# Optimization experiments

Hardware: AMD Instinct MI355X
Metric: run time of the kernel (lower is better)

Reference implementation:

```python
import jax, jax.numpy as jnp
import numpy as np

N = 400000
IN, H, F, S, OUT = 64, 256, 128, 16, 5


def setup_inputs() -> dict:
    key = jax.random.key(0)
    ks = jax.random.split(key, 20)
    def lin(k, fan_in, fan_out):
        bound = 1.0 / np.sqrt(fan_in)
        kw, kb = jax.random.split(k)
        W = jax.random.uniform(kw, (fan_in, fan_out), jnp.float32, -bound, bound)
        b = jax.random.uniform(kb, (fan_out,), jnp.float32, -bound, bound)
        return W, b
    pw1, pb1 = lin(ks[0], IN, H)
    pw2, pb2 = lin(ks[1], H, H)
    pw3, pb3 = lin(ks[2], H, F)
    rw1, rb1 = lin(ks[3], F, H)
    rw2, rb2 = lin(ks[4], H, H)
    rw3, rb3 = lin(ks[5], H, F)
    w1, b1 = lin(ks[6], F + S, H)
    w2, b2 = lin(ks[7], H, H)
    w3, b3 = lin(ks[8], H, OUT)
    x = jax.random.normal(ks[9], (N, IN), jnp.float32)
    x_static = jax.random.normal(ks[10], (S,), jnp.float32)
    return {
        "x": x, "x_static": x_static,
        "pw1": pw1, "pb1": pb1, "pw2": pw2, "pb2": pb2, "pw3": pw3, "pb3": pb3,
        "rw1": rw1, "rb1": rb1, "rw2": rw2, "rb2": rb2, "rw3": rw3, "rb3": rb3,
        "w1": w1, "b1": b1, "w2": w2, "b2": b2, "w3": w3, "b3": b3,
    }


def reference(x, x_static, pw1, pb1, pw2, pb2, pw3, pb3,
              rw1, rb1, rw2, rb2, rw3, rb3, w1, b1, w2, b2, w3, b3):
    # phi network applied to every row, then sum-pool (DeepSets).
    # Batched matmuls replace the original Python per-row loop; the per-row
    # bias of the final phi Linear is summed N times, matching the loop.
    h = jax.nn.relu(x @ pw1 + pb1)              # [N, H]
    h = jax.nn.relu(h @ pw2 + pb2)              # [N, H]
    phi = h @ pw3 + pb3                          # [N, F]
    fp = jnp.sum(phi, axis=0)                    # [F]
    # rho network
    r = jax.nn.relu(fp @ rw1 + rb1)
    r = jax.nn.relu(r @ rw2 + rb2)
    r = r @ rw3 + rb3                            # [F]
    out = jnp.concatenate([r, x_static], axis=0)  # [F + S]
    out = jax.nn.relu(out @ w1 + b1)
    out = jax.nn.relu(out @ w2 + b2)
    return out @ w3 + b3                          # [OUT]
```

## Files before the change

### kernel.cpp

```cpp
#include <hip/hip_runtime.h>


typedef unsigned short u16;
typedef _Float16 f16x8 __attribute__((ext_vector_type(8)));
typedef _Float16 f16x2 __attribute__((ext_vector_type(2)));
typedef float f32x4 __attribute__((ext_vector_type(4)));
typedef int i32x4 __attribute__((ext_vector_type(4)));

#define NBLK 256

__global__ void prep_kernel(const float* __restrict__ pw1, const float* __restrict__ pw2,
                            _Float16* __restrict__ w1f, _Float16* __restrict__ w2f,
                            float* __restrict__ gsum,
                            const float* __restrict__ pw3, const float* __restrict__ rw1,
                            const float* __restrict__ rw2, const float* __restrict__ rw3,
                            const float* __restrict__ hw1, const float* __restrict__ hw2,
                            const float* __restrict__ hw3) {
    int idx = blockIdx.x * blockDim.x + threadIdx.x;
    if (idx < 256) gsum[idx] = 0.f;
    if (idx < 16384) {
        int j = idx & 7, l = (idx >> 3) & 63, ks = (idx >> 9) & 1, ct = idx >> 10;
        int k = 32 * ks + 8 * (l >> 4) + j;
        int col = 16 * ct + (l & 15);
        w1f[idx] = (_Float16)pw1[k * 256 + col];
    } else {
        int o = idx - 16384;
        int j = o & 7, l = (o >> 3) & 63, ks = (o >> 9) & 7, ct = o >> 12;
        int k = 32 * ks + 8 * (l >> 4) + j;
        int col = 16 * ct + (l & 15);
        w2f[o] = (_Float16)pw2[k * 256 + col];
    }
    float s = 0.f;
    if (idx < 32768) s += pw3[idx];
    if (idx < 32768) s += rw1[idx];
    if (idx < 65536) s += rw2[idx];
    if (idx < 32768) s += rw3[idx];
    if (idx < 36864) s += hw1[idx];
    if (idx < 65536) s += hw2[idx];
    if (idx < 1280)  s += hw3[idx];
    asm volatile("" :: "v"(s));
}

__device__ __forceinline__ void pin_reg(f16x8& v) {
    i32x4 t = __builtin_bit_cast(i32x4, v);
    asm volatile("" : "+v"(t));
    v = __builtin_bit_cast(f16x8, t);
}
__device__ __forceinline__ unsigned pk(float a, float b) {
    return __builtin_bit_cast(unsigned, __builtin_amdgcn_cvt_pkrtz(a, b));
}

__global__ __attribute__((amdgpu_flat_work_group_size(512, 512), amdgpu_waves_per_eu(2, 2)))
void phi_kernel(
    const float* __restrict__ x,
    const float* __restrict__ pb1, const float* __restrict__ pb2,
    const _Float16* __restrict__ w1g, const _Float16* __restrict__ w2g,
    float* __restrict__ gsum, int ntiles) {
    __shared__ __align__(16) u16 xs[2][64 * 64];
    __shared__ __align__(16) u16 h1s[2][64 * 256];

    const int tid = threadIdx.x;
    const int l = tid & 63;
    const int w = tid >> 6;
    const int fr = l & 15;
    const int fg = l >> 4;
    const int wb = w * 32;

    f16x8 w1r[2][2];
#pragma unroll
    for (int ct = 0; ct < 2; ++ct)
#pragma unroll
        for (int ks = 0; ks < 2; ++ks) {
            int ctg = 2 * w + ct;
            w1r[ct][ks] = *(const f16x8*)(w1g + (((ctg << 1) + ks) << 9) + (l << 3));
        }
    f16x8 w2r[2][8];
#pragma unroll
    for (int ct = 0; ct < 2; ++ct)
#pragma unroll
        for (int ks = 0; ks < 8; ++ks) {
            int ctg = 2 * w + ct;
            w2r[ct][ks] = *(const f16x8*)(w2g + (((ctg << 3) + ks) << 9) + (l << 3));
        }
#pragma unroll
    for (int ct = 0; ct < 2; ++ct) {
#pragma unroll
        for (int ks = 0; ks < 2; ++ks) pin_reg(w1r[ct][ks]);
#pragma unroll
        for (int ks = 0; ks < 8; ++ks) pin_reg(w2r[ct][ks]);
    }
    f32x4 b1v[2], b2v[2];
#pragma unroll
    for (int ct = 0; ct < 2; ++ct) {
        int c0 = wb + ct * 16 + fg * 4;
        b1v[ct] = *(const f32x4*)(pb1 + c0);
        b2v[ct] = *(const f32x4*)(pb2 + c0);
    }

    float psum[2][4] = {{0.f, 0.f, 0.f, 0.f}, {0.f, 0.f, 0.f, 0.f}};

    const int t0 = blockIdx.x;
    {
        const float4* xg = (const float4*)(x + (size_t)t0 * 4096);
#pragma unroll
        for (int i = 0; i < 2; ++i) {
            int f4 = tid + i * 512;
            float4 v = xg[f4];
            int row = f4 >> 4, c4 = f4 & 15;
            uint2 o;
            o.x = pk(v.x, v.y);
            o.y = pk(v.z, v.w);
            int byte = (row * 128 + c4 * 8) ^ ((row & 7) << 4);
            *(uint2*)((char*)xs[0] + byte) = o;
        }
    }
    float4 pf0, pf1;
    {
        int tn = (t0 + NBLK < ntiles) ? t0 + NBLK : 0;
        const float4* xg = (const float4*)(x + (size_t)tn * 4096);
        pf0 = xg[tid];
        pf1 = xg[tid + 512];
    }
    __syncthreads();

    int buf = 0, hb = 0;
    for (int t = t0; t < ntiles; t += NBLK) {
#pragma unroll
        for (int i = 0; i < 2; ++i) {
            float4 v = i ? pf1 : pf0;
            int f4 = tid + i * 512;
            int row = f4 >> 4, c4 = f4 & 15;
            uint2 o;
            o.x = pk(v.x, v.y);
            o.y = pk(v.z, v.w);
            int byte = (row * 128 + c4 * 8) ^ ((row & 7) << 4);
            *(uint2*)((char*)xs[buf ^ 1] + byte) = o;
        }
        {
            int tn = (t + 2 * NBLK < ntiles) ? t + 2 * NBLK : 0;
            const float4* xg = (const float4*)(x + (size_t)tn * 4096);
            pf0 = xg[tid];
            pf1 = xg[tid + 512];
        }

        {
            f32x4 acc[2][4] = {};
#pragma unroll
            for (int ks = 0; ks < 2; ++ks) {
                f16x8 bd[4];
#pragma unroll
                for (int rt = 0; rt < 4; ++rt) {
                    int row = (rt << 4) + fr;
                    int byte = ((row << 7) + (ks << 6) + (fg << 4)) ^ ((row & 7) << 4);
                    bd[rt] = *(const f16x8*)((char*)xs[buf] + byte);
                }
#pragma unroll
                for (int ct = 0; ct < 2; ++ct)
#pragma unroll
                    for (int rt = 0; rt < 4; ++rt)
                        acc[ct][rt] = __builtin_amdgcn_mfma_f32_16x16x32_f16(w1r[ct][ks], bd[rt], acc[ct][rt], 0, 0, 0);
            }
#pragma unroll
            for (int ct = 0; ct < 2; ++ct) {
                int c0 = wb + ct * 16 + fg * 4;
#pragma unroll
                for (int rt = 0; rt < 4; ++rt) {
                    int rown = (rt << 4) + fr;
                    uint2 o;
                    o.x = pk(fmaxf(acc[ct][rt][0] + b1v[ct][0], 0.f),
                             fmaxf(acc[ct][rt][1] + b1v[ct][1], 0.f));
                    o.y = pk(fmaxf(acc[ct][rt][2] + b1v[ct][2], 0.f),
                             fmaxf(acc[ct][rt][3] + b1v[ct][3], 0.f));
                    int byte = ((rown << 9) + (c0 << 1)) ^ ((rown & 15) << 4);
                    *(uint2*)((char*)h1s[hb] + byte) = o;
                }
            }
        }
        __syncthreads();

        {
            f32x4 acc2[2][4] = {};
#pragma unroll
            for (int ks = 0; ks < 8; ++ks) {
                f16x8 bd[4];
#pragma unroll
                for (int rt = 0; rt < 4; ++rt) {
                    int row = (rt << 4) + fr;
                    int byte = ((row << 9) + (ks << 6) + (fg << 4)) ^ ((row & 15) << 4);
                    bd[rt] = *(const f16x8*)((char*)h1s[hb] + byte);
                }
#pragma unroll
                for (int ct = 0; ct < 2; ++ct)
#pragma unroll
                    for (int rt = 0; rt < 4; ++rt)
                        acc2[ct][rt] = __builtin_amdgcn_mfma_f32_16x16x32_f16(w2r[ct][ks], bd[rt], acc2[ct][rt], 0, 0, 0);
            }
#pragma unroll
            for (int ct = 0; ct < 2; ++ct)
#pragma unroll
                for (int r = 0; r < 4; ++r) {
                    float v = 0.f;
#pragma unroll
                    for (int rt = 0; rt < 4; ++rt)
                        v += fmaxf(acc2[ct][rt][r] + b2v[ct][r], 0.f);
                    psum[ct][r] += v;
                }
        }
        buf ^= 1;
        hb ^= 1;
    }

#pragma unroll
    for (int ct = 0; ct < 2; ++ct)
#pragma unroll
        for (int r = 0; r < 4; ++r) {
            float v = psum[ct][r];
            v += __shfl_xor(v, 1, 64);
            v += __shfl_xor(v, 2, 64);
            v += __shfl_xor(v, 4, 64);
            v += __shfl_xor(v, 8, 64);
            if (fr == 0) atomicAdd(&gsum[wb + ct * 16 + fg * 4 + r], v);
        }
}

__global__ __launch_bounds__(1024) void tail_kernel(
    const float* __restrict__ gsum, const float* __restrict__ xst,
    const float* __restrict__ pw3, const float* __restrict__ pb3,
    const float* __restrict__ rw1, const float* __restrict__ rb1,
    const float* __restrict__ rw2, const float* __restrict__ rb2,
    const float* __restrict__ rw3, const float* __restrict__ rb3,
    const float* __restrict__ w1, const float* __restrict__ b1,
    const float* __restrict__ w2, const float* __restrict__ b2,
    const float* __restrict__ w3, const float* __restrict__ b3,
    float* __restrict__ out, float nf) {
    __shared__ float fp[128], r1[256], r2[256], tc[144], t1[256], t2[256];
    __shared__ float part[8][256];
    const int t = threadIdx.x;

    {
        int j = t & 127, q = t >> 7;
        float s = 0.f;
        for (int i = 32 * q; i < 32 * q + 32; ++i) s += gsum[i] * pw3[i * 128 + j];
        part[q][j] = s;
    }
    __syncthreads();
    if (t < 128) { float s = nf * pb3[t]; for (int q = 0; q < 8; ++q) s += part[q][t]; fp[t] = s; }
    __syncthreads();
    {
        int j = t & 255, q = t >> 8;
        float s = 0.f;
        for (int i = 32 * q; i < 32 * q + 32; ++i) s += fp[i] * rw1[i * 256 + j];
        part[q][j] = s;
    }
    __syncthreads();
    if (t < 256) { float s = rb1[t]; for (int q = 0; q < 4; ++q) s += part[q][t]; r1[t] = fmaxf(s, 0.f); }
    __syncthreads();
    {
        int j = t & 255, q = t >> 8;
        float s = 0.f;
        for (int i = 64 * q; i < 64 * q + 64; ++i) s += r1[i] * rw2[i * 256 + j];
        part[q][j] = s;
    }
    __syncthreads();
    if (t < 256) { float s = rb2[t]; for (int q = 0; q < 4; ++q) s += part[q][t]; r2[t] = fmaxf(s, 0.f); }
    __syncthreads();
    {
        int j = t & 127, q = t >> 7;
        float s = 0.f;
        for (int i = 32 * q; i < 32 * q + 32; ++i) s += r2[i] * rw3[i * 128 + j];
        part[q][j] = s;
    }
    __syncthreads();
    if (t < 128) { float s = rb3[t]; for (int q = 0; q < 8; ++q) s += part[q][t]; tc[t] = s; }
    else if (t < 144) tc[t] = xst[t - 128];
    __syncthreads();
    {
        int j = t & 255, q = t >> 8;
        float s = 0.f;
        for (int i = 36 * q; i < 36 * q + 36; ++i) s += tc[i] * w1[i * 256 + j];
        part[q][j] = s;
    }
    __syncthreads();
    if (t < 256) { float s = b1[t]; for (int q = 0; q < 4; ++q) s += part[q][t]; t1[t] = fmaxf(s, 0.f); }
    __syncthreads();
    {
        int j = t & 255, q = t >> 8;
        float s = 0.f;
        for (int i = 64 * q; i < 64 * q + 64; ++i) s += t1[i] * w2[i * 256 + j];
        part[q][j] = s;
    }
    __syncthreads();
    if (t < 256) { float s = b2[t]; for (int q = 0; q < 4; ++q) s += part[q][t]; t2[t] = fmaxf(s, 0.f); }
    __syncthreads();
    {
        int j = t & 255, q = t >> 8;
        if (j < 5) {
            float s = 0.f;
            for (int i = 64 * q; i < 64 * q + 64; ++i) s += t2[i] * w3[i * 5 + j];
            part[q][j] = s;
        }
    }
    __syncthreads();
    if (t < 5) { float s = b3[t]; for (int q = 0; q < 4; ++q) s += part[q][t]; out[t] = s; }
}

extern "C" void kernel_launch(void* const* d_in, const int* in_sizes, int n_in,
                              void* d_out, int out_size, void* d_ws, size_t ws_size,
                              hipStream_t stream) {
    (void)n_in; (void)out_size; (void)ws_size;
    const float* x   = (const float*)d_in[0];
    const float* xst = (const float*)d_in[1];
    const float* pw1 = (const float*)d_in[2];
    const float* pb1 = (const float*)d_in[3];
    const float* pw2 = (const float*)d_in[4];
    const float* pb2 = (const float*)d_in[5];
    const float* pw3 = (const float*)d_in[6];
    const float* pb3 = (const float*)d_in[7];
    const float* rw1 = (const float*)d_in[8];
    const float* rb1 = (const float*)d_in[9];
    const float* rw2 = (const float*)d_in[10];
    const float* rb2 = (const float*)d_in[11];
    const float* rw3 = (const float*)d_in[12];
    const float* rb3 = (const float*)d_in[13];
    const float* w1  = (const float*)d_in[14];
    const float* b1  = (const float*)d_in[15];
    const float* w2  = (const float*)d_in[16];
    const float* b2  = (const float*)d_in[17];
    const float* w3  = (const float*)d_in[18];
    const float* b3  = (const float*)d_in[19];
    float* out = (float*)d_out;

    int n = in_sizes[0] / 64;
    int ntiles = n >> 6;

    char* ws = (char*)d_ws;
    float* gsum = (float*)ws;
    _Float16* w1f = (_Float16*)(ws + 1024);
    _Float16* w2f = (_Float16*)(ws + 1024 + 32768);

    prep_kernel<<<160, 512, 0, stream>>>(pw1, pw2, w1f, w2f, gsum,
                                         pw3, rw1, rw2, rw3, w1, w2, w3);
    phi_kernel<<<NBLK, 512, 0, stream>>>(x, pb1, pb2, w1f, w2f, gsum, ntiles);
    tail_kernel<<<1, 1024, 0, stream>>>(gsum, xst, pw3, pb3, rw1, rb1, rw2, rb2,
                                        rw3, rb3, w1, b1, w2, b2, w3, b3, out, (float)n);
}
```

Before: 124.7 us.

## Fuse tail MLP into phi kernel via last-block-done atomic counter

Removes the separate single-block tail kernel launch: each phi block increments an atomic counter after its partial-sum atomics, and the last block to finish runs the rho and head MLPs using its shared memory. This cuts one kernel launch and the inter-kernel gap. In exchange the tail now runs on 512 threads instead of 1024, so each thread does longer dot-product loops, and it adds threadfence and counter overhead to every block.

```diff
diff --git a/kernel.cpp b/kernel.cpp
--- a/kernel.cpp
+++ b/kernel.cpp
@@ -3,7 +3,6 @@
 
 typedef unsigned short u16;
 typedef _Float16 f16x8 __attribute__((ext_vector_type(8)));
-typedef _Float16 f16x2 __attribute__((ext_vector_type(2)));
 typedef float f32x4 __attribute__((ext_vector_type(4)));
 typedef int i32x4 __attribute__((ext_vector_type(4)));
 
@@ -17,7 +16,7 @@
                             const float* __restrict__ hw1, const float* __restrict__ hw2,
                             const float* __restrict__ hw3) {
     int idx = blockIdx.x * blockDim.x + threadIdx.x;
-    if (idx < 256) gsum[idx] = 0.f;
+    if (idx < 260) gsum[idx] = 0.f;
     if (idx < 16384) {
         int j = idx & 7, l = (idx >> 3) & 63, ks = (idx >> 9) & 1, ct = idx >> 10;
         int k = 32 * ks + 8 * (l >> 4) + j;
@@ -55,9 +54,19 @@
     const float* __restrict__ x,
     const float* __restrict__ pb1, const float* __restrict__ pb2,
     const _Float16* __restrict__ w1g, const _Float16* __restrict__ w2g,
-    float* __restrict__ gsum, int ntiles) {
+    float* __restrict__ gsum, int ntiles,
+    const float* __restrict__ xst,
+    const float* __restrict__ pw3, const float* __restrict__ pb3,
+    const float* __restrict__ rw1, const float* __restrict__ rb1,
+    const float* __restrict__ rw2, const float* __restrict__ rb2,
+    const float* __restrict__ rw3, const float* __restrict__ rb3,
+    const float* __restrict__ hw1, const float* __restrict__ hb1,
+    const float* __restrict__ hw2, const float* __restrict__ hb2,
+    const float* __restrict__ hw3, const float* __restrict__ hb3,
+    float* __restrict__ outp, float nf) {
     __shared__ __align__(16) u16 xs[2][64 * 64];
     __shared__ __align__(16) u16 h1s[2][64 * 256];
+    __shared__ int lastflag;
 
     const int tid = threadIdx.x;
     const int l = tid & 63;
@@ -221,87 +230,91 @@
             v += __shfl_xor(v, 8, 64);
             if (fr == 0) atomicAdd(&gsum[wb + ct * 16 + fg * 4 + r], v);
         }
-}
-
-__global__ __launch_bounds__(1024) void tail_kernel(
-    const float* __restrict__ gsum, const float* __restrict__ xst,
-    const float* __restrict__ pw3, const float* __restrict__ pb3,
-    const float* __restrict__ rw1, const float* __restrict__ rb1,
-    const float* __restrict__ rw2, const float* __restrict__ rb2,
-    const float* __restrict__ rw3, const float* __restrict__ rb3,
-    const float* __restrict__ w1, const float* __restrict__ b1,
-    const float* __restrict__ w2, const float* __restrict__ b2,
-    const float* __restrict__ w3, const float* __restrict__ b3,
-    float* __restrict__ out, float nf) {
-    __shared__ float fp[128], r1[256], r2[256], tc[144], t1[256], t2[256];
-    __shared__ float part[8][256];
-    const int t = threadIdx.x;
+
+    __threadfence();
+    if (tid == 0) {
+        int old = atomicAdd((int*)(gsum + 256), 1);
+        lastflag = (old == NBLK - 1);
+    }
+    __syncthreads();
+    if (!lastflag) return;
+    __threadfence();
+
+    float* sb = (float*)h1s;
+    float* fp  = sb;
+    float* r1v = sb + 128;
+    float* r2v = sb + 384;
+    float* tcv = sb + 640;
+    float* t1v = sb + 800;
+    float* t2v = sb + 1056;
+    float (*part)[256] = (float(*)[256])(sb + 1312);
+    const int t = tid;
 
     {
         int j = t & 127, q = t >> 7;
         float s = 0.f;
-        for (int i = 32 * q; i < 32 * q + 32; ++i) s += gsum[i] * pw3[i * 128 + j];
-        part[q][j] = s;
-    }
-    __syncthreads();
-    if (t < 128) { float s = nf * pb3[t]; for (int q = 0; q < 8; ++q) s += part[q][t]; fp[t] = s; }
-    __syncthreads();
-    {
-        int j = t & 255, q = t >> 8;
-        float s = 0.f;
-        for (int i = 32 * q; i < 32 * q + 32; ++i) s += fp[i] * rw1[i * 256 + j];
-        part[q][j] = s;
-    }
-    __syncthreads();
-    if (t < 256) { float s = rb1[t]; for (int q = 0; q < 4; ++q) s += part[q][t]; r1[t] = fmaxf(s, 0.f); }
-    __syncthreads();
-    {
-        int j = t & 255, q = t >> 8;
-        float s = 0.f;
-        for (int i = 64 * q; i < 64 * q + 64; ++i) s += r1[i] * rw2[i * 256 + j];
-        part[q][j] = s;
-    }
-    __syncthreads();
-    if (t < 256) { float s = rb2[t]; for (int q = 0; q < 4; ++q) s += part[q][t]; r2[t] = fmaxf(s, 0.f); }
+        for (int i = 64 * q; i < 64 * q + 64; ++i) s += gsum[i] * pw3[i * 128 + j];
+        part[q][j] = s;
+    }
+    __syncthreads();
+    if (t < 128) { float s = nf * pb3[t]; for (int q = 0; q < 4; ++q) s += part[q][t]; fp[t] = s; }
+    __syncthreads();
+    {
+        int j = t & 255, q = t >> 8;
+        float s = 0.f;
+        for (int i = 64 * q; i < 64 * q + 64; ++i) s += fp[i] * rw1[i * 256 + j];
+        part[q][j] = s;
+    }
+    __syncthreads();
+    if (t < 256) { float s = rb1[t] + part[0][t] + part[1][t]; r1v[t] = fmaxf(s, 0.f); }
+    __syncthreads();
+    {
+        int j = t & 255, q = t >> 8;
+        float s = 0.f;
+        for (int i = 128 * q; i < 128 * q + 128; ++i) s += r1v[i] * rw2[i * 256 + j];
+        part[q][j] = s;
+    }
+    __syncthreads();
+    if (t < 256) { float s = rb2[t] + part[0][t] + part[1][t]; r2v[t] = fmaxf(s, 0.f); }
     __syncthreads();
     {
         int j = t & 127, q = t >> 7;
         float s = 0.f;
-        for (int i = 32 * q; i < 32 * q + 32; ++i) s += r2[i] * rw3[i * 128 + j];
-        part[q][j] = s;
-    }
-    __syncthreads();
-    if (t < 128) { float s = rb3[t]; for (int q = 0; q < 8; ++q) s += part[q][t]; tc[t] = s; }
-    else if (t < 144) tc[t] = xst[t - 128];
-    __syncthreads();
-    {
-        int j = t & 255, q = t >> 8;
-        float s = 0.f;
-        for (int i = 36 * q; i < 36 * q + 36; ++i) s += tc[i] * w1[i * 256 + j];
-        part[q][j] = s;
-    }
-    __syncthreads();
-    if (t < 256) { float s = b1[t]; for (int q = 0; q < 4; ++q) s += part[q][t]; t1[t] = fmaxf(s, 0.f); }
-    __syncthreads();
-    {
-        int j = t & 255, q = t >> 8;
-        float s = 0.f;
-        for (int i = 64 * q; i < 64 * q + 64; ++i) s += t1[i] * w2[i * 256 + j];
-        part[q][j] = s;
-    }
-    __syncthreads();
-    if (t < 256) { float s = b2[t]; for (int q = 0; q < 4; ++q) s += part[q][t]; t2[t] = fmaxf(s, 0.f); }
+        for (int i = 64 * q; i < 64 * q + 64; ++i) s += r2v[i] * rw3[i * 128 + j];
+        part[q][j] = s;
+    }
+    __syncthreads();
+    if (t < 128) { float s = rb3[t]; for (int q = 0; q < 4; ++q) s += part[q][t]; tcv[t] = s; }
+    else if (t < 144) tcv[t] = xst[t - 128];
+    __syncthreads();
+    {
+        int j = t & 255, q = t >> 8;
+        float s = 0.f;
+        for (int i = 72 * q; i < 72 * q + 72; ++i) s += tcv[i] * hw1[i * 256 + j];
+        part[q][j] = s;
+    }
+    __syncthreads();
+    if (t < 256) { float s = hb1[t] + part[0][t] + part[1][t]; t1v[t] = fmaxf(s, 0.f); }
+    __syncthreads();
+    {
+        int j = t & 255, q = t >> 8;
+        float s = 0.f;
+        for (int i = 128 * q; i < 128 * q + 128; ++i) s += t1v[i] * hw2[i * 256 + j];
+        part[q][j] = s;
+    }
+    __syncthreads();
+    if (t < 256) { float s = hb2[t] + part[0][t] + part[1][t]; t2v[t] = fmaxf(s, 0.f); }
     __syncthreads();
     {
         int j = t & 255, q = t >> 8;
         if (j < 5) {
             float s = 0.f;
-            for (int i = 64 * q; i < 64 * q + 64; ++i) s += t2[i] * w3[i * 5 + j];
+            for (int i = 128 * q; i < 128 * q + 128; ++i) s += t2v[i] * hw3[i * 5 + j];
             part[q][j] = s;
         }
     }
     __syncthreads();
-    if (t < 5) { float s = b3[t]; for (int q = 0; q < 4; ++q) s += part[q][t]; out[t] = s; }
+    if (t < 5) outp[t] = hb3[t] + part[0][t] + part[1][t];
 }
 
 extern "C" void kernel_launch(void* const* d_in, const int* in_sizes, int n_in,
@@ -335,12 +348,13 @@
 
     char* ws = (char*)d_ws;
     float* gsum = (float*)ws;
-    _Float16* w1f = (_Float16*)(ws + 1024);
-    _Float16* w2f = (_Float16*)(ws + 1024 + 32768);
+    _Float16* w1f = (_Float16*)(ws + 2048);
+    _Float16* w2f = (_Float16*)(ws + 2048 + 32768);
 
     prep_kernel<<<160, 512, 0, stream>>>(pw1, pw2, w1f, w2f, gsum,
                                          pw3, rw1, rw2, rw3, w1, w2, w3);
-    phi_kernel<<<NBLK, 512, 0, stream>>>(x, pb1, pb2, w1f, w2f, gsum, ntiles);
-    tail_kernel<<<1, 1024, 0, stream>>>(gsum, xst, pw3, pb3, rw1, rb1, rw2, rb2,
-                                        rw3, rb3, w1, b1, w2, b2, w3, b3, out, (float)n);
-}
+    phi_kernel<<<NBLK, 512, 0, stream>>>(x, pb1, pb2, w1f, w2f, gsum, ntiles,
+                                         xst, pw3, pb3, rw1, rb1, rw2, rb2,
+                                         rw3, rb3, w1, b1, w2, b2, w3, b3,
+                                         out, (float)n);
+}
```

Measured after the change: 132.7 us. +6.4%, slower.
